# Kernel optimization log

Hardware: AMD Instinct MI355X
Metric: run time of the kernel (lower is better)

Reference implementation:

```python
import jax, jax.numpy as jnp
import numpy as np

NE, NM, D = 10000, 2048, 128
LEVELS = 6  # levels arg 5 -> self.levels = 6 relation types


def setup_inputs() -> dict:
    key = jax.random.key(0)
    ks = jax.random.split(key, 9)
    s = 0.05
    return {
        "emb_entity": jax.random.normal(ks[0], (1, NE, D), jnp.float32),
        "emb_mole": jax.random.normal(ks[1], (1, NM, D), jnp.float32),
        "entity_mole_weight": jax.random.uniform(ks[2], (NE, NM), jnp.float32),
        "W1": jax.random.normal(ks[3], (LEVELS, D, D), jnp.float32) * s,
        "root1": jax.random.normal(ks[4], (D, D), jnp.float32) * s,
        "b1": jax.random.normal(ks[5], (D,), jnp.float32) * s,
        "W2": jax.random.normal(ks[6], (LEVELS, D, D), jnp.float32) * s,
        "root2": jax.random.normal(ks[7], (D, D), jnp.float32) * s,
        "b2": jax.random.normal(ks[8], (D,), jnp.float32) * s,
    }


def reference(emb_entity, emb_mole, entity_mole_weight, W1, root1, b1, W2, root2, b2):
    x_e = emb_entity[0]  # [NE, D]
    x_m = emb_mole[0]    # [NM, D]
    # weight w in (i/LEVELS, (i+1)/LEVELS]  <=>  ceil(w*LEVELS) - 1 == i ; only i=1..LEVELS-1 form edges
    lev = jnp.ceil(entity_mole_weight * LEVELS).astype(jnp.int32) - 1  # [NE, NM]

    def rel_agg(x_src, W):
        # RGCN mean aggregation per relation type (edges Mole -> Entity), summed over relations
        out = jnp.zeros((x_e.shape[0], W.shape[-1]), x_src.dtype)
        for r in range(1, LEVELS):
            mask = (lev == r).astype(x_src.dtype)          # [NE, NM] relation-r adjacency
            cnt = mask.sum(axis=1, keepdims=True)          # in-degree per entity for relation r
            inv = jnp.where(cnt > 0, 1.0 / cnt, 0.0)
            out = out + ((mask @ x_src) * inv) @ W[r]      # mean message then relation transform
        return out

    # conv1 over homogeneous graph [Entity; Mole]; moles receive no edges -> root+bias only
    e1 = x_e @ root1 + rel_agg(x_m, W1) + b1
    m1 = x_m @ root1 + b1
    e1 = jax.nn.relu(e1)
    m1 = jax.nn.relu(m1)
    # conv2; only the entity slice of the output is returned
    e2 = e1 @ root2 + rel_agg(m1, W2) + b2
    return e2[None]  # [1, NE, D]
```

## Files before the change

### kernel.cpp

```cpp
#include <hip/hip_runtime.h>
#include <stdint.h>


#define NE 10000
#define NM 2048
#define NEPAD 10112
#define MB128 79
#define KSPLIT 16

typedef short bf8_t __attribute__((ext_vector_type(8)));
typedef float f16f  __attribute__((ext_vector_type(16)));

__device__ __forceinline__ uint16_t f2bf(float f){
  uint32_t u = __float_as_uint(f);
  u += 0x7FFFu + ((u >> 16) & 1u);
  return (uint16_t)(u >> 16);
}

__device__ __forceinline__ f16f mfma32(bf8_t a, bf8_t b, f16f c){
  return __builtin_amdgcn_mfma_f32_32x32x16_bf16(a, b, c, 0, 0, 0);
}

__global__ __launch_bounds__(256) void k_init(
    const float* __restrict__ root1, const float* __restrict__ root2,
    const float* __restrict__ W1, const float* __restrict__ W2,
    uint16_t* __restrict__ r1t, uint16_t* __restrict__ r2t,
    uint16_t* __restrict__ w1t, uint16_t* __restrict__ w2t,
    const float* __restrict__ w, const float* __restrict__ xe,
    uint32_t* __restrict__ levq, float* __restrict__ inv,
    uint16_t* __restrict__ xebf){
  int t = threadIdx.x;
  if (blockIdx.x < 48){
    int idx = blockIdx.x*4096 + t;
    #pragma unroll
    for (int it = 0; it < 16; it++, idx += 256){
      int slab = idx >> 14;
      int pos  = idx & 16383;
      int d = pos >> 7, k = pos & 127;
      float v; uint16_t* dst;
      if (slab == 0)      { v = root1[k*128 + d]; dst = r1t; }
      else if (slab == 1) { v = root2[k*128 + d]; dst = r2t; }
      else if (slab < 7)  { v = W1[(slab-1)*16384 + k*128 + d]; dst = w1t + (slab-2)*16384; }
      else                { v = W2[(slab-6)*16384 + k*128 + d]; dst = w2t + (slab-7)*16384; }
      dst[pos] = f2bf(v);
    }
    return;
  }
  int brow = (blockIdx.x - 48) * 32;
  int rloc = t >> 3, p = t & 7;
  int row = brow + rloc;
  bool active = row < NE;
  const float* wr = w + (size_t)row * NM;
  unsigned long long cnt = 0ull;
  __shared__ uint32_t tile[32][33];

  for (int cp = 0; cp < 8; cp++){
    uint32_t packs[4];
    #pragma unroll
    for (int q = 0; q < 4; q++){
      int gck = cp*32 + p + 8*q;
      uint32_t L = 0;
      if (active){
        const float4* f = (const float4*)(wr + gck*8);
        float4 f0 = f[0], f1 = f[1];
        float wv[8] = {f0.x,f0.y,f0.z,f0.w, f1.x,f1.y,f1.z,f1.w};
        #pragma unroll
        for (int e = 0; e < 8; e++){
          int s = (int)ceilf(wv[e]*6.0f);
          if (s >= 2) cnt += 1ull << (12*(s-2));
          L |= (uint32_t)s << (4*e);
        }
      }
      packs[q] = L;
    }
    __syncthreads();
    #pragma unroll
    for (int q = 0; q < 4; q++) tile[p + 8*q][rloc] = packs[q];
    __syncthreads();
    int ckk = t >> 3;
    int r4  = (t & 7) * 4;
    size_t base = (size_t)(cp*32 + ckk) * NEPAD + brow + r4;
    *(uint4*)(levq + base) = make_uint4(tile[ckk][r4], tile[ckk][r4+1],
                                        tile[ckk][r4+2], tile[ckk][r4+3]);
  }

  unsigned long long c = cnt;
  c += __shfl_xor(c, 1);
  c += __shfl_xor(c, 2);
  c += __shfl_xor(c, 4);
  if (p == 0 && row < NEPAD){
    if (active){
      inv[row*8 + 0] = 0.f; inv[row*8 + 6] = 0.f; inv[row*8 + 7] = 0.f;
      #pragma unroll
      for (int r = 1; r <= 5; r++){
        uint32_t cc = (uint32_t)((c >> (12*(r-1))) & 0xFFFull);
        inv[row*8 + r] = cc ? 1.0f/(float)cc : 0.f;
      }
    } else {
      #pragma unroll
      for (int i = 0; i < 8; i++) inv[row*8 + i] = 0.f;
    }
  }

  int f0i = p * 16;
  if (active){
    union { uint16_t u[16]; uint4 q[2]; } ub;
    #pragma unroll
    for (int j = 0; j < 4; j++){
      float4 a = *(const float4*)(xe + (size_t)row*128 + f0i + j*4);
      ub.u[j*4+0]=f2bf(a.x); ub.u[j*4+1]=f2bf(a.y); ub.u[j*4+2]=f2bf(a.z); ub.u[j*4+3]=f2bf(a.w);
    }
    *(uint4*)(xebf + (size_t)row*128 + f0i)     = ub.q[0];
    *(uint4*)(xebf + (size_t)row*128 + f0i + 8) = ub.q[1];
  } else if (row < NEPAD){
    uint4 z = make_uint4(0,0,0,0);
    *(uint4*)(xebf + (size_t)row*128 + f0i)     = z;
    *(uint4*)(xebf + (size_t)row*128 + f0i + 8) = z;
  }
}

__global__ __launch_bounds__(256) void k_gemm(
    const float* __restrict__ Af, const uint16_t* __restrict__ Bm,
    const uint16_t* __restrict__ Bz, const float* __restrict__ bias,
    uint16_t* __restrict__ m1out, uint16_t* __restrict__ zpk){
  int tid = threadIdx.x;
  int lane = tid & 63, wid = tid >> 6;
  int l31 = lane & 31, g = lane >> 5;
  int by = blockIdx.y;
  bool m1path = (by == 0);
  int r = by - 1;
  const uint16_t* B = m1path ? Bm : (Bz + (size_t)r*16384);
  int arow = blockIdx.x*128 + wid*32 + l31;

  f16f acc[4];
  #pragma unroll
  for (int n = 0; n < 4; n++)
    #pragma unroll
    for (int i = 0; i < 16; i++) acc[n][i] = 0.f;

  #pragma unroll
  for (int ksI = 0; ksI < 8; ksI++){
    int k0 = ksI*16 + g*8;
    const float* ap = Af + (size_t)arow*128 + k0;
    float4 f0 = *(const float4*)ap;
    float4 f1 = *(const float4*)(ap + 4);
    union { uint16_t u[8]; bf8_t v; } ua;
    ua.u[0]=f2bf(f0.x); ua.u[1]=f2bf(f0.y); ua.u[2]=f2bf(f0.z); ua.u[3]=f2bf(f0.w);
    ua.u[4]=f2bf(f1.x); ua.u[5]=f2bf(f1.y); ua.u[6]=f2bf(f1.z); ua.u[7]=f2bf(f1.w);
    #pragma unroll
    for (int n = 0; n < 4; n++){
      bf8_t b = *(const bf8_t*)(B + (size_t)(n*32 + l31)*128 + k0);
      acc[n] = mfma32(ua.v, b, acc[n]);
    }
  }
  #pragma unroll
  for (int n = 0; n < 4; n++){
    int colg = n*32 + l31;
    float bv = m1path ? bias[colg] : 0.f;
    #pragma unroll
    for (int v = 0; v < 16; v++){
      int rowl = (v&3) + 8*(v>>2) + 4*g;
      int rg = blockIdx.x*128 + wid*32 + rowl;
      float val = acc[n][v];
      if (m1path){
        m1out[(size_t)rg*128 + colg] = f2bf(fmaxf(val + bv, 0.f));
      } else {
        int pos = ((rg & 1) << 2) | ((rg & 7) >> 1);
        zpk[(size_t)(r*256 + (rg>>3))*1024 + colg*8 + pos] = f2bf(val);
      }
    }
  }
}

template<bool S16, bool ROOT>
__device__ __forceinline__ void conv_core(
    const uint32_t* __restrict__ levq, const float* __restrict__ inv,
    const uint16_t* __restrict__ zpk, const uint16_t* __restrict__ aroot,
    const uint16_t* __restrict__ rt,
    uint16_t* __restrict__ p16, float* __restrict__ p32,
    int tid){
  int lane = tid & 63, wid = tid >> 6;
  int l31 = lane & 31, g = lane >> 5;
  int wm = wid >> 1, wn = wid & 1;
  int bx = blockIdx.x;
  int brow = bx*128;
  int ks = blockIdx.y;
  int kc0 = ks*16;
  int rowA = brow + wm*64 + l31;
  int rowB = rowA + 32;
  int colb = wn*64;

  uint32_t LA[8], LB[8];
  #pragma unroll
  for (int j = 0; j < 8; j++){
    int kt = kc0 + ((j + bx) & 7)*2 + g;
    LA[j] = levq[(size_t)kt*NEPAD + rowA];
    LB[j] = levq[(size_t)kt*NEPAD + rowB];
  }

  uint32_t tlo[2][5], thi[2][5];
  #pragma unroll
  for (int mt = 0; mt < 2; mt++){
    int rg = mt ? rowB : rowA;
    #pragma unroll
    for (int r = 1; r <= 5; r++){
      uint32_t bits = (uint32_t)f2bf(inv[(size_t)rg*8 + r]);
      int sh = 8*((r+1)&3);
      tlo[mt][r-1] = (bits & 0xFFu) << sh;
      thi[mt][r-1] = (bits >> 8)    << sh;
    }
  }

  f16f acc[2][2];
  #pragma unroll
  for (int a0=0;a0<2;a0++)
    #pragma unroll
    for (int b0=0;b0<2;b0++)
      #pragma unroll
      for (int i=0;i<16;i++) acc[a0][b0][i]=0.f;

  if (ROOT && ks < 8){
    int k0 = ks*16 + g*8;
    bf8_t a0 = *(const bf8_t*)(aroot + (size_t)rowA*128 + k0);
    bf8_t a1 = *(const bf8_t*)(aroot + (size_t)rowB*128 + k0);
    #pragma unroll
    for (int nt = 0; nt < 2; nt++){
      bf8_t rb = *(const bf8_t*)(rt + (size_t)(colb + nt*32 + l31)*128 + k0);
      acc[0][nt] = mfma32(a0, rb, acc[0][nt]);
      acc[1][nt] = mfma32(a1, rb, acc[1][nt]);
    }
  }

  #pragma unroll
  for (int kk = 0; kk < 8; kk++){
    int kt = kc0 + ((kk + bx) & 7)*2 + g;
    uint32_t sxA = LA[kk] & 0x0F0F0F0Fu, syA = (LA[kk] >> 4) & 0x0F0F0F0Fu;
    uint32_t sxB = LB[kk] & 0x0F0F0F0Fu, syB = (LB[kk] >> 4) & 0x0F0F0F0Fu;
    const uint16_t* zb = zpk + (size_t)kt*1024 + (size_t)(colb + l31)*8;
    #pragma unroll
    for (int r = 1; r <= 5; r++){
      const uint16_t* zr = zb + (size_t)(r-1)*262144;
      bf8_t bn0 = *(const bf8_t*)(zr);
      bf8_t bn1 = *(const bf8_t*)(zr + 256);
      #pragma unroll
      for (int mt = 0; mt < 2; mt++){
        uint32_t sx = mt ? sxB : sxA;
        uint32_t sy = mt ? syB : syA;
        uint32_t TL = tlo[mt][r-1], TH = thi[mt][r-1];
        uint32_t pl, ph, ql, qh;
        if (r < 3){
          pl = __builtin_amdgcn_perm(0u, TL, sx);
          ph = __builtin_amdgcn_perm(0u, TH, sx);
          ql = __builtin_amdgcn_perm(0u, TL, sy);
          qh = __builtin_amdgcn_perm(0u, TH, sy);
        } else {
          pl = __builtin_amdgcn_perm(TL, 0u, sx);
          ph = __builtin_amdgcn_perm(TH, 0u, sx);
          ql = __builtin_amdgcn_perm(TL, 0u, sy);
          qh = __builtin_amdgcn_perm(TH, 0u, sy);
        }
        union { uint32_t u[4]; bf8_t v; } A;
        A.u[0] = __builtin_amdgcn_perm(ph, pl, 0x05010400u);
        A.u[1] = __builtin_amdgcn_perm(ph, pl, 0x07030602u);
        A.u[2] = __builtin_amdgcn_perm(qh, ql, 0x05010400u);
        A.u[3] = __builtin_amdgcn_perm(qh, ql, 0x07030602u);
        acc[mt][0] = mfma32(A.v, bn0, acc[mt][0]);
        acc[mt][1] = mfma32(A.v, bn1, acc[mt][1]);
      }
    }
  }

  if (S16){
    uint16_t* dst = p16 + (size_t)ks*NEPAD*128;
    #pragma unroll
    for (int mt = 0; mt < 2; mt++){
      #pragma unroll
      for (int nt = 0; nt < 2; nt++){
        int colg = colb + nt*32 + l31;
        #pragma unroll
        for (int v = 0; v < 16; v++){
          int rowl = (v&3) + 8*(v>>2) + 4*g;
          dst[(size_t)(brow + wm*64 + mt*32 + rowl)*128 + colg] = f2bf(acc[mt][nt][v]);
        }
      }
    }
  } else {
    #pragma unroll
    for (int mt = 0; mt < 2; mt++){
      #pragma unroll
      for (int nt = 0; nt < 2; nt++){
        int colg = colb + nt*32 + l31;
        #pragma unroll
        for (int v = 0; v < 16; v++){
          int rowl = (v&3) + 8*(v>>2) + 4*g;
          unsafeAtomicAdd(&p32[(size_t)(brow + wm*64 + mt*32 + rowl)*128 + colg],
                          acc[mt][nt][v]);
        }
      }
    }
  }
}

template<bool S16>
__global__ __launch_bounds__(256, 3) void k_convA(
    const uint32_t* __restrict__ levq, const float* __restrict__ inv,
    const uint16_t* __restrict__ zpk, const uint16_t* __restrict__ aroot,
    const uint16_t* __restrict__ rt,
    const uint16_t* __restrict__ gA, const uint16_t* __restrict__ gB,
    uint16_t* __restrict__ gOut,
    uint16_t* __restrict__ p16, float* __restrict__ p32){
  int tid = threadIdx.x;
  int lane = tid & 63, wid = tid >> 6;
  int l31 = lane & 31, g = lane >> 5;

  if (blockIdx.x >= MB128){
    int b = blockIdx.y*5 + (blockIdx.x - MB128);
    int r = b >> 4;
    int rowb = (b & 15)*128 + wid*32;
    int arow = rowb + l31;
    const uint16_t* B = gB + (size_t)r*16384;
    f16f acc[4];
    #pragma unroll
    for (int n = 0; n < 4; n++)
      #pragma unroll
      for (int i = 0; i < 16; i++) acc[n][i] = 0.f;
    #pragma unroll
    for (int ksI = 0; ksI < 8; ksI++){
      int k0 = ksI*16 + g*8;
      bf8_t a = *(const bf8_t*)(gA + (size_t)arow*128 + k0);
      #pragma unroll
      for (int n = 0; n < 4; n++){
        bf8_t bb = *(const bf8_t*)(B + (size_t)(n*32 + l31)*128 + k0);
        acc[n] = mfma32(a, bb, acc[n]);
      }
    }
    #pragma unroll
    for (int n = 0; n < 4; n++){
      int colg = n*32 + l31;
      #pragma unroll
      for (int v = 0; v < 16; v++){
        int rowl = (v&3) + 8*(v>>2) + 4*g;
        int rg = rowb + rowl;
        int pos = ((rg & 1) << 2) | ((rg & 7) >> 1);
        gOut[(size_t)(r*256 + (rg>>3))*1024 + colg*8 + pos] = f2bf(acc[n][v]);
      }
    }
    return;
  }
  conv_core<S16, true>(levq, inv, zpk, aroot, rt, p16, p32, tid);
}

template<bool S16>
__global__ __launch_bounds__(256, 3) void k_convB(
    const uint32_t* __restrict__ levq, const float* __restrict__ inv,
    const uint16_t* __restrict__ zpk,
    const uint16_t* __restrict__ pA16, const float* __restrict__ pA32,
    const uint16_t* __restrict__ rt, const float* __restrict__ b1,
    uint16_t* __restrict__ pB16, float* __restrict__ pB32,
    float* __restrict__ rootslab){
  __shared__ uint16_t e1s[128*136];
  int tid = threadIdx.x;
  int lane = tid & 63, wid = tid >> 6;
  int l31 = lane & 31, g = lane >> 5;

  if (blockIdx.x >= MB128){
    int rid = blockIdx.y*5 + (blockIdx.x - MB128);
    if (rid >= MB128) return;
    #pragma unroll
    for (int c = 0; c < 8; c++){
      int eo = c*2048 + tid*8;
      size_t base = (size_t)rid*16384 + eo;
      int col = eo & 127;
      float s[8];
      float4 bv0 = *(const float4*)(b1 + col);
      float4 bv1 = *(const float4*)(b1 + col + 4);
      s[0]=bv0.x; s[1]=bv0.y; s[2]=bv0.z; s[3]=bv0.w;
      s[4]=bv1.x; s[5]=bv1.y; s[6]=bv1.z; s[7]=bv1.w;
      if (S16){
        #pragma unroll
        for (int sl = 0; sl < KSPLIT; sl++){
          union { uint4 q; uint16_t h[8]; } u;
          u.q = *(const uint4*)(pA16 + (size_t)sl*NEPAD*128 + base);
          #pragma unroll
          for (int j = 0; j < 8; j++) s[j] += __uint_as_float(((uint32_t)u.h[j]) << 16);
        }
      } else {
        #pragma unroll
        for (int j = 0; j < 8; j += 4){
          float4 v = *(const float4*)(pA32 + base + j);
          s[j] += v.x; s[j+1] += v.y; s[j+2] += v.z; s[j+3] += v.w;
        }
      }
      union { uint16_t u[8]; uint4 q; } ub;
      #pragma unroll
      for (int j = 0; j < 8; j++) ub.u[j] = f2bf(fmaxf(s[j], 0.f));
      int row = eo >> 7;
      *(uint4*)(&e1s[row*136 + col]) = ub.q;
    }
    __syncthreads();
    f16f racc[4];
    #pragma unroll
    for (int n = 0; n < 4; n++)
      #pragma unroll
      for (int i = 0; i < 16; i++) racc[n][i] = 0.f;
    #pragma unroll
    for (int kk = 0; kk < 8; kk++){
      int k0 = kk*16 + g*8;
      bf8_t a = *(const bf8_t*)(&e1s[(wid*32 + l31)*136 + k0]);
      #pragma unroll
      for (int n = 0; n < 4; n++){
        bf8_t b = *(const bf8_t*)(rt + (size_t)(n*32 + l31)*128 + k0);
        racc[n] = mfma32(a, b, racc[n]);
      }
    }
    #pragma unroll
    for (int n = 0; n < 4; n++){
      int colg = n*32 + l31;
      #pragma unroll
      for (int v = 0; v < 16; v++){
        int rowl = (v&3) + 8*(v>>2) + 4*g;
        rootslab[(size_t)(rid*128 + wid*32 + rowl)*128 + colg] = racc[n][v];
      }
    }
    return;
  }
  conv_core<S16, false>(levq, inv, zpk, (const uint16_t*)nullptr, rt, pB16, pB32, tid);
}

template<bool S16>
__global__ __launch_bounds__(256) void k_red2(
    const uint16_t* __restrict__ pB16, const float* __restrict__ pB32,
    const float* __restrict__ rootslab, const float* __restrict__ b2,
    float* __restrict__ out){
  size_t idx8 = ((size_t)blockIdx.x*256 + threadIdx.x) * 8;
  if (idx8 >= (size_t)NE*128) return;
  int col = (int)(idx8 & 127);
  float s[8];
  float4 bv0 = *(const float4*)(b2 + col);
  float4 bv1 = *(const float4*)(b2 + col + 4);
  s[0]=bv0.x; s[1]=bv0.y; s[2]=bv0.z; s[3]=bv0.w;
  s[4]=bv1.x; s[5]=bv1.y; s[6]=bv1.z; s[7]=bv1.w;
  float4 r0 = *(const float4*)(rootslab + idx8);
  float4 r1 = *(const float4*)(rootslab + idx8 + 4);
  s[0]+=r0.x; s[1]+=r0.y; s[2]+=r0.z; s[3]+=r0.w;
  s[4]+=r1.x; s[5]+=r1.y; s[6]+=r1.z; s[7]+=r1.w;
  if (S16){
    #pragma unroll
    for (int sl = 0; sl < KSPLIT; sl++){
      union { uint4 q; uint16_t h[8]; } u;
      u.q = *(const uint4*)(pB16 + (size_t)sl*NEPAD*128 + idx8);
      #pragma unroll
      for (int j = 0; j < 8; j++) s[j] += __uint_as_float(((uint32_t)u.h[j]) << 16);
    }
  } else {
    #pragma unroll
    for (int j = 0; j < 8; j += 4){
      float4 v = *(const float4*)(pB32 + idx8 + j);
      s[j] += v.x; s[j+1] += v.y; s[j+2] += v.z; s[j+3] += v.w;
    }
  }
  *(float4*)(out + idx8)     = make_float4(s[0], s[1], s[2], s[3]);
  *(float4*)(out + idx8 + 4) = make_float4(s[4], s[5], s[6], s[7]);
}

extern "C" void kernel_launch(void* const* d_in, const int* in_sizes, int n_in,
                              void* d_out, int out_size, void* d_ws, size_t ws_size,
                              hipStream_t stream){
  const float* xe  = (const float*)d_in[0];
  const float* xm  = (const float*)d_in[1];
  const float* w   = (const float*)d_in[2];
  const float* W1  = (const float*)d_in[3];
  const float* r1  = (const float*)d_in[4];
  const float* b1  = (const float*)d_in[5];
  const float* W2  = (const float*)d_in[6];
  const float* r2  = (const float*)d_in[7];
  const float* b2  = (const float*)d_in[8];
  float* out = (float*)d_out;
  char* ws = (char*)d_ws;

  constexpr size_t OFF_INV  = 0;
  constexpr size_t OFF_XEBF = OFF_INV  + (size_t)NEPAD*8*4;
  constexpr size_t OFF_M1   = OFF_XEBF + (size_t)NEPAD*128*2;
  constexpr size_t OFF_Z1   = OFF_M1   + (size_t)NM*128*2;
  constexpr size_t OFF_Z2   = OFF_Z1   + (size_t)5*NM*128*2;
  constexpr size_t OFF_R1T  = OFF_Z2   + (size_t)5*NM*128*2;
  constexpr size_t OFF_R2T  = OFF_R1T  + 128*128*2;
  constexpr size_t OFF_W1T  = OFF_R2T  + 128*128*2;
  constexpr size_t OFF_W2T  = OFF_W1T  + (size_t)5*128*128*2;
  constexpr size_t OFF_LEVQ = OFF_W2T  + (size_t)5*128*128*2;
  constexpr size_t OFF_PA   = OFF_LEVQ + (size_t)256*NEPAD*4;
  constexpr size_t SLAB16   = (size_t)NEPAD*128*2;
  constexpr size_t SLABF    = (size_t)NEPAD*128*4;
  constexpr size_t OFF_PB   = OFF_PA   + (size_t)KSPLIT*SLAB16;
  constexpr size_t OFF_ROOT = OFF_PB   + (size_t)KSPLIT*SLAB16;
  constexpr size_t NEED_A   = OFF_ROOT + SLABF;
  constexpr size_t OFF_PB_B   = OFF_PA + SLABF;
  constexpr size_t OFF_ROOT_B = OFF_PB_B + SLABF;
  constexpr size_t NEED_B     = OFF_ROOT_B + SLABF;

  float*    inv  = (float*)   (ws + OFF_INV);
  uint16_t* xebf = (uint16_t*)(ws + OFF_XEBF);
  uint16_t* m1   = (uint16_t*)(ws + OFF_M1);
  uint16_t* z1   = (uint16_t*)(ws + OFF_Z1);
  uint16_t* z2   = (uint16_t*)(ws + OFF_Z2);
  uint16_t* r1t  = (uint16_t*)(ws + OFF_R1T);
  uint16_t* r2t  = (uint16_t*)(ws + OFF_R2T);
  uint16_t* w1t  = (uint16_t*)(ws + OFF_W1T);
  uint16_t* w2t  = (uint16_t*)(ws + OFF_W2T);
  uint32_t* levq = (uint32_t*)(ws + OFF_LEVQ);

  bool tierA = (ws_size >= NEED_A);

  hipLaunchKernelGGL(k_init, dim3(48 + NEPAD/32), dim3(256), 0, stream,
                     r1, r2, W1, W2, r1t, r2t, w1t, w2t,
                     w, xe, levq, inv, xebf);
  hipLaunchKernelGGL(k_gemm, dim3(16,6), dim3(256), 0, stream,
                     xm, r1t, w1t, b1, m1, z1);
  if (tierA){
    uint16_t* pA   = (uint16_t*)(ws + OFF_PA);
    uint16_t* pB   = (uint16_t*)(ws + OFF_PB);
    float*    root = (float*)   (ws + OFF_ROOT);
    hipLaunchKernelGGL((k_convA<true>), dim3(MB128 + 5, KSPLIT), dim3(256), 0, stream,
                       levq, inv, z1, xebf, r1t, m1, w2t, z2,
                       pA, (float*)nullptr);
    hipLaunchKernelGGL((k_convB<true>), dim3(MB128 + 5, KSPLIT), dim3(256), 0, stream,
                       levq, inv, z2, pA, (const float*)nullptr, r2t, b1,
                       pB, (float*)nullptr, root);
    hipLaunchKernelGGL((k_red2<true>), dim3((NE*128 + 2047)/2048), dim3(256), 0, stream,
                       pB, (const float*)nullptr, root, b2, out);
  } else {
    float* pA   = (float*)(ws + OFF_PA);
    float* pB   = (float*)(ws + OFF_PB_B);
    float* root = (float*)(ws + OFF_ROOT_B);
    hipMemsetAsync(pA, 0, SLABF, stream);
    hipMemsetAsync(pB, 0, SLABF, stream);
    hipLaunchKernelGGL((k_convA<false>), dim3(MB128 + 5, KSPLIT), dim3(256), 0, stream,
                       levq, inv, z1, xebf, r1t, m1, w2t, z2,
                       (uint16_t*)nullptr, pA);
    hipLaunchKernelGGL((k_convB<false>), dim3(MB128 + 5, KSPLIT), dim3(256), 0, stream,
                       levq, inv, z2, (const uint16_t*)nullptr, pA, r2t, b1,
                       (uint16_t*)nullptr, pB, root);
    hipLaunchKernelGGL((k_red2<false>), dim3((NE*128 + 2047)/2048), dim3(256), 0, stream,
                       (const uint16_t*)nullptr, pB, root, b2, out);
  }
}
```

Before: 127.9 us.

## Fuse mole GEMM into init kernel and read fp32 weights directly

Drops the separate weight-transpose/bf16 conversion pass and the standalone k_gemm launch. The mole-side GEMMs (m1 and the z1 relation products) now run as extra blocks inside k_init. All consumers read fp32 root/W matrices straight from the inputs, gathering strided columns and converting to bf16 on the fly. The intent is to save one kernel launch and a pass over weight memory. In exchange, B-operand loads become strided scalar reads with per-element conversion. The conv kernels also get a lower occupancy hint (2 instead of 3) and drop the per-block k-tile rotation.

```diff
diff --git a/kernel.cpp b/kernel.cpp
--- a/kernel.cpp
+++ b/kernel.cpp
@@ -22,31 +22,69 @@
 }
 
 __global__ __launch_bounds__(256) void k_init(
-    const float* __restrict__ root1, const float* __restrict__ root2,
-    const float* __restrict__ W1, const float* __restrict__ W2,
-    uint16_t* __restrict__ r1t, uint16_t* __restrict__ r2t,
-    uint16_t* __restrict__ w1t, uint16_t* __restrict__ w2t,
     const float* __restrict__ w, const float* __restrict__ xe,
+    const float* __restrict__ xm, const float* __restrict__ root1,
+    const float* __restrict__ W1, const float* __restrict__ b1,
     uint32_t* __restrict__ levq, float* __restrict__ inv,
-    uint16_t* __restrict__ xebf){
+    uint16_t* __restrict__ xebf, uint16_t* __restrict__ m1,
+    uint16_t* __restrict__ z1){
   int t = threadIdx.x;
-  if (blockIdx.x < 48){
-    int idx = blockIdx.x*4096 + t;
-    #pragma unroll
-    for (int it = 0; it < 16; it++, idx += 256){
-      int slab = idx >> 14;
-      int pos  = idx & 16383;
-      int d = pos >> 7, k = pos & 127;
-      float v; uint16_t* dst;
-      if (slab == 0)      { v = root1[k*128 + d]; dst = r1t; }
-      else if (slab == 1) { v = root2[k*128 + d]; dst = r2t; }
-      else if (slab < 7)  { v = W1[(slab-1)*16384 + k*128 + d]; dst = w1t + (slab-2)*16384; }
-      else                { v = W2[(slab-6)*16384 + k*128 + d]; dst = w2t + (slab-7)*16384; }
-      dst[pos] = f2bf(v);
+  int lane = t & 63, wid = t >> 6;
+  int l31 = lane & 31, g = lane >> 5;
+
+  if (blockIdx.x >= 316){
+    int gb = blockIdx.x - 316;
+    int gbx = gb & 15, gby = gb >> 4;
+    bool m1path = (gby == 0);
+    const float* Bsrc = m1path ? root1 : (W1 + (size_t)gby*16384);
+    int arow = gbx*128 + wid*32 + l31;
+
+    f16f acc[4];
+    #pragma unroll
+    for (int n = 0; n < 4; n++)
+      #pragma unroll
+      for (int i = 0; i < 16; i++) acc[n][i] = 0.f;
+
+    #pragma unroll
+    for (int ksI = 0; ksI < 8; ksI++){
+      int k0 = ksI*16 + g*8;
+      const float* ap = xm + (size_t)arow*128 + k0;
+      float4 f0 = *(const float4*)ap;
+      float4 f1 = *(const float4*)(ap + 4);
+      union { uint16_t u[8]; bf8_t v; } ua;
+      ua.u[0]=f2bf(f0.x); ua.u[1]=f2bf(f0.y); ua.u[2]=f2bf(f0.z); ua.u[3]=f2bf(f0.w);
+      ua.u[4]=f2bf(f1.x); ua.u[5]=f2bf(f1.y); ua.u[6]=f2bf(f1.z); ua.u[7]=f2bf(f1.w);
+      #pragma unroll
+      for (int n = 0; n < 4; n++){
+        int d = n*32 + l31;
+        union { uint16_t u[8]; bf8_t v; } ub;
+        #pragma unroll
+        for (int e = 0; e < 8; e++)
+          ub.u[e] = f2bf(Bsrc[(size_t)(k0+e)*128 + d]);
+        acc[n] = mfma32(ua.v, ub.v, acc[n]);
+      }
+    }
+    #pragma unroll
+    for (int n = 0; n < 4; n++){
+      int colg = n*32 + l31;
+      float bv = m1path ? b1[colg] : 0.f;
+      #pragma unroll
+      for (int v = 0; v < 16; v++){
+        int rowl = (v&3) + 8*(v>>2) + 4*g;
+        int rg = gbx*128 + wid*32 + rowl;
+        float val = acc[n][v];
+        if (m1path){
+          m1[(size_t)rg*128 + colg] = f2bf(fmaxf(val + bv, 0.f));
+        } else {
+          int pos = ((rg & 1) << 2) | ((rg & 7) >> 1);
+          z1[(size_t)((gby-1)*256 + (rg>>3))*1024 + colg*8 + pos] = f2bf(val);
+        }
+      }
     }
     return;
   }
-  int brow = (blockIdx.x - 48) * 32;
+
+  int brow = blockIdx.x * 32;
   int rloc = t >> 3, p = t & 7;
   int row = brow + rloc;
   bool active = row < NE;
@@ -119,71 +157,16 @@
   }
 }
 
-__global__ __launch_bounds__(256) void k_gemm(
-    const float* __restrict__ Af, const uint16_t* __restrict__ Bm,
-    const uint16_t* __restrict__ Bz, const float* __restrict__ bias,
-    uint16_t* __restrict__ m1out, uint16_t* __restrict__ zpk){
-  int tid = threadIdx.x;
-  int lane = tid & 63, wid = tid >> 6;
-  int l31 = lane & 31, g = lane >> 5;
-  int by = blockIdx.y;
-  bool m1path = (by == 0);
-  int r = by - 1;
-  const uint16_t* B = m1path ? Bm : (Bz + (size_t)r*16384);
-  int arow = blockIdx.x*128 + wid*32 + l31;
-
-  f16f acc[4];
-  #pragma unroll
-  for (int n = 0; n < 4; n++)
-    #pragma unroll
-    for (int i = 0; i < 16; i++) acc[n][i] = 0.f;
-
-  #pragma unroll
-  for (int ksI = 0; ksI < 8; ksI++){
-    int k0 = ksI*16 + g*8;
-    const float* ap = Af + (size_t)arow*128 + k0;
-    float4 f0 = *(const float4*)ap;
-    float4 f1 = *(const float4*)(ap + 4);
-    union { uint16_t u[8]; bf8_t v; } ua;
-    ua.u[0]=f2bf(f0.x); ua.u[1]=f2bf(f0.y); ua.u[2]=f2bf(f0.z); ua.u[3]=f2bf(f0.w);
-    ua.u[4]=f2bf(f1.x); ua.u[5]=f2bf(f1.y); ua.u[6]=f2bf(f1.z); ua.u[7]=f2bf(f1.w);
-    #pragma unroll
-    for (int n = 0; n < 4; n++){
-      bf8_t b = *(const bf8_t*)(B + (size_t)(n*32 + l31)*128 + k0);
-      acc[n] = mfma32(ua.v, b, acc[n]);
-    }
-  }
-  #pragma unroll
-  for (int n = 0; n < 4; n++){
-    int colg = n*32 + l31;
-    float bv = m1path ? bias[colg] : 0.f;
-    #pragma unroll
-    for (int v = 0; v < 16; v++){
-      int rowl = (v&3) + 8*(v>>2) + 4*g;
-      int rg = blockIdx.x*128 + wid*32 + rowl;
-      float val = acc[n][v];
-      if (m1path){
-        m1out[(size_t)rg*128 + colg] = f2bf(fmaxf(val + bv, 0.f));
-      } else {
-        int pos = ((rg & 1) << 2) | ((rg & 7) >> 1);
-        zpk[(size_t)(r*256 + (rg>>3))*1024 + colg*8 + pos] = f2bf(val);
-      }
-    }
-  }
-}
-
 template<bool S16, bool ROOT>
 __device__ __forceinline__ void conv_core(
     const uint32_t* __restrict__ levq, const float* __restrict__ inv,
     const uint16_t* __restrict__ zpk, const uint16_t* __restrict__ aroot,
-    const uint16_t* __restrict__ rt,
-    uint16_t* __restrict__ p16, float* __restrict__ p32,
-    int tid){
+    const float* __restrict__ rootf,
+    uint16_t* __restrict__ p16, float* __restrict__ p32, int tid){
   int lane = tid & 63, wid = tid >> 6;
   int l31 = lane & 31, g = lane >> 5;
   int wm = wid >> 1, wn = wid & 1;
-  int bx = blockIdx.x;
-  int brow = bx*128;
+  int brow = blockIdx.x*128;
   int ks = blockIdx.y;
   int kc0 = ks*16;
   int rowA = brow + wm*64 + l31;
@@ -192,10 +175,10 @@
 
   uint32_t LA[8], LB[8];
   #pragma unroll
-  for (int j = 0; j < 8; j++){
-    int kt = kc0 + ((j + bx) & 7)*2 + g;
-    LA[j] = levq[(size_t)kt*NEPAD + rowA];
-    LB[j] = levq[(size_t)kt*NEPAD + rowB];
+  for (int kk = 0; kk < 8; kk++){
+    int kt = kc0 + kk*2 + g;
+    LA[kk] = levq[(size_t)kt*NEPAD + rowA];
+    LB[kk] = levq[(size_t)kt*NEPAD + rowB];
   }
 
   uint32_t tlo[2][5], thi[2][5];
@@ -225,15 +208,19 @@
     bf8_t a1 = *(const bf8_t*)(aroot + (size_t)rowB*128 + k0);
     #pragma unroll
     for (int nt = 0; nt < 2; nt++){
-      bf8_t rb = *(const bf8_t*)(rt + (size_t)(colb + nt*32 + l31)*128 + k0);
-      acc[0][nt] = mfma32(a0, rb, acc[0][nt]);
-      acc[1][nt] = mfma32(a1, rb, acc[1][nt]);
+      int d = colb + nt*32 + l31;
+      union { uint16_t u[8]; bf8_t v; } ub;
+      #pragma unroll
+      for (int e = 0; e < 8; e++)
+        ub.u[e] = f2bf(rootf[(size_t)(k0+e)*128 + d]);
+      acc[0][nt] = mfma32(a0, ub.v, acc[0][nt]);
+      acc[1][nt] = mfma32(a1, ub.v, acc[1][nt]);
     }
   }
 
   #pragma unroll
   for (int kk = 0; kk < 8; kk++){
-    int kt = kc0 + ((kk + bx) & 7)*2 + g;
+    int kt = kc0 + kk*2 + g;
     uint32_t sxA = LA[kk] & 0x0F0F0F0Fu, syA = (LA[kk] >> 4) & 0x0F0F0F0Fu;
     uint32_t sxB = LB[kk] & 0x0F0F0F0Fu, syB = (LB[kk] >> 4) & 0x0F0F0F0Fu;
     const uint16_t* zb = zpk + (size_t)kt*1024 + (size_t)(colb + l31)*8;
@@ -302,23 +289,23 @@
 }
 
 template<bool S16>
-__global__ __launch_bounds__(256, 3) void k_convA(
+__global__ __launch_bounds__(256, 2) void k_convA(
     const uint32_t* __restrict__ levq, const float* __restrict__ inv,
-    const uint16_t* __restrict__ zpk, const uint16_t* __restrict__ aroot,
-    const uint16_t* __restrict__ rt,
-    const uint16_t* __restrict__ gA, const uint16_t* __restrict__ gB,
-    uint16_t* __restrict__ gOut,
+    const uint16_t* __restrict__ z1, const uint16_t* __restrict__ xebf,
+    const float* __restrict__ root1,
+    const uint16_t* __restrict__ m1, const float* __restrict__ W2,
+    uint16_t* __restrict__ z2,
     uint16_t* __restrict__ p16, float* __restrict__ p32){
   int tid = threadIdx.x;
   int lane = tid & 63, wid = tid >> 6;
   int l31 = lane & 31, g = lane >> 5;
 
   if (blockIdx.x >= MB128){
-    int b = blockIdx.y*5 + (blockIdx.x - MB128);
-    int r = b >> 4;
-    int rowb = (b & 15)*128 + wid*32;
+    int fb = blockIdx.y*5 + (blockIdx.x - MB128);
+    int r = fb >> 4;
+    int rowb = (fb & 15)*128 + wid*32;
     int arow = rowb + l31;
-    const uint16_t* B = gB + (size_t)r*16384;
+    const float* Bsrc = W2 + (size_t)(r+1)*16384;
     f16f acc[4];
     #pragma unroll
     for (int n = 0; n < 4; n++)
@@ -327,11 +314,15 @@
     #pragma unroll
     for (int ksI = 0; ksI < 8; ksI++){
       int k0 = ksI*16 + g*8;
-      bf8_t a = *(const bf8_t*)(gA + (size_t)arow*128 + k0);
+      bf8_t a = *(const bf8_t*)(m1 + (size_t)arow*128 + k0);
       #pragma unroll
       for (int n = 0; n < 4; n++){
-        bf8_t bb = *(const bf8_t*)(B + (size_t)(n*32 + l31)*128 + k0);
-        acc[n] = mfma32(a, bb, acc[n]);
+        int d = n*32 + l31;
+        union { uint16_t u[8]; bf8_t v; } ub;
+        #pragma unroll
+        for (int e = 0; e < 8; e++)
+          ub.u[e] = f2bf(Bsrc[(size_t)(k0+e)*128 + d]);
+        acc[n] = mfma32(a, ub.v, acc[n]);
       }
     }
     #pragma unroll
@@ -342,20 +333,20 @@
         int rowl = (v&3) + 8*(v>>2) + 4*g;
         int rg = rowb + rowl;
         int pos = ((rg & 1) << 2) | ((rg & 7) >> 1);
-        gOut[(size_t)(r*256 + (rg>>3))*1024 + colg*8 + pos] = f2bf(acc[n][v]);
+        z2[(size_t)(r*256 + (rg>>3))*1024 + colg*8 + pos] = f2bf(acc[n][v]);
       }
     }
     return;
   }
-  conv_core<S16, true>(levq, inv, zpk, aroot, rt, p16, p32, tid);
+  conv_core<S16, true>(levq, inv, z1, xebf, root1, p16, p32, tid);
 }
 
 template<bool S16>
-__global__ __launch_bounds__(256, 3) void k_convB(
+__global__ __launch_bounds__(256, 2) void k_convB(
     const uint32_t* __restrict__ levq, const float* __restrict__ inv,
-    const uint16_t* __restrict__ zpk,
+    const uint16_t* __restrict__ z2,
     const uint16_t* __restrict__ pA16, const float* __restrict__ pA32,
-    const uint16_t* __restrict__ rt, const float* __restrict__ b1,
+    const float* __restrict__ root2, const float* __restrict__ b1,
     uint16_t* __restrict__ pB16, float* __restrict__ pB32,
     float* __restrict__ rootslab){
   __shared__ uint16_t e1s[128*136];
@@ -409,8 +400,12 @@
       bf8_t a = *(const bf8_t*)(&e1s[(wid*32 + l31)*136 + k0]);
       #pragma unroll
       for (int n = 0; n < 4; n++){
-        bf8_t b = *(const bf8_t*)(rt + (size_t)(n*32 + l31)*128 + k0);
-        racc[n] = mfma32(a, b, racc[n]);
+        int d = n*32 + l31;
+        union { uint16_t u[8]; bf8_t v; } ub;
+        #pragma unroll
+        for (int e = 0; e < 8; e++)
+          ub.u[e] = f2bf(root2[(size_t)(k0+e)*128 + d]);
+        racc[n] = mfma32(a, ub.v, racc[n]);
       }
     }
     #pragma unroll
@@ -424,7 +419,8 @@
     }
     return;
   }
-  conv_core<S16, false>(levq, inv, zpk, (const uint16_t*)nullptr, rt, pB16, pB32, tid);
+  conv_core<S16, false>(levq, inv, z2, (const uint16_t*)nullptr,
+                        (const float*)nullptr, pB16, pB32, tid);
 }
 
 template<bool S16>
@@ -483,11 +479,7 @@
   constexpr size_t OFF_M1   = OFF_XEBF + (size_t)NEPAD*128*2;
   constexpr size_t OFF_Z1   = OFF_M1   + (size_t)NM*128*2;
   constexpr size_t OFF_Z2   = OFF_Z1   + (size_t)5*NM*128*2;
-  constexpr size_t OFF_R1T  = OFF_Z2   + (size_t)5*NM*128*2;
-  constexpr size_t OFF_R2T  = OFF_R1T  + 128*128*2;
-  constexpr size_t OFF_W1T  = OFF_R2T  + 128*128*2;
-  constexpr size_t OFF_W2T  = OFF_W1T  + (size_t)5*128*128*2;
-  constexpr size_t OFF_LEVQ = OFF_W2T  + (size_t)5*128*128*2;
+  constexpr size_t OFF_LEVQ = OFF_Z2   + (size_t)5*NM*128*2;
   constexpr size_t OFF_PA   = OFF_LEVQ + (size_t)256*NEPAD*4;
   constexpr size_t SLAB16   = (size_t)NEPAD*128*2;
   constexpr size_t SLABF    = (size_t)NEPAD*128*4;
@@ -496,35 +488,26 @@
   constexpr size_t NEED_A   = OFF_ROOT + SLABF;
   constexpr size_t OFF_PB_B   = OFF_PA + SLABF;
   constexpr size_t OFF_ROOT_B = OFF_PB_B + SLABF;
-  constexpr size_t NEED_B     = OFF_ROOT_B + SLABF;
 
   float*    inv  = (float*)   (ws + OFF_INV);
   uint16_t* xebf = (uint16_t*)(ws + OFF_XEBF);
   uint16_t* m1   = (uint16_t*)(ws + OFF_M1);
   uint16_t* z1   = (uint16_t*)(ws + OFF_Z1);
   uint16_t* z2   = (uint16_t*)(ws + OFF_Z2);
-  uint16_t* r1t  = (uint16_t*)(ws + OFF_R1T);
-  uint16_t* r2t  = (uint16_t*)(ws + OFF_R2T);
-  uint16_t* w1t  = (uint16_t*)(ws + OFF_W1T);
-  uint16_t* w2t  = (uint16_t*)(ws + OFF_W2T);
   uint32_t* levq = (uint32_t*)(ws + OFF_LEVQ);
 
   bool tierA = (ws_size >= NEED_A);
 
-  hipLaunchKernelGGL(k_init, dim3(48 + NEPAD/32), dim3(256), 0, stream,
-                     r1, r2, W1, W2, r1t, r2t, w1t, w2t,
-                     w, xe, levq, inv, xebf);
-  hipLaunchKernelGGL(k_gemm, dim3(16,6), dim3(256), 0, stream,
-                     xm, r1t, w1t, b1, m1, z1);
+  hipLaunchKernelGGL(k_init, dim3(316 + 96), dim3(256), 0, stream,
+                     w, xe, xm, r1, W1, b1, levq, inv, xebf, m1, z1);
   if (tierA){
     uint16_t* pA   = (uint16_t*)(ws + OFF_PA);
     uint16_t* pB   = (uint16_t*)(ws + OFF_PB);
     float*    root = (float*)   (ws + OFF_ROOT);
     hipLaunchKernelGGL((k_convA<true>), dim3(MB128 + 5, KSPLIT), dim3(256), 0, stream,
-                       levq, inv, z1, xebf, r1t, m1, w2t, z2,
-                       pA, (float*)nullptr);
+                       levq, inv, z1, xebf, r1, m1, W2, z2, pA, (float*)nullptr);
     hipLaunchKernelGGL((k_convB<true>), dim3(MB128 + 5, KSPLIT), dim3(256), 0, stream,
-                       levq, inv, z2, pA, (const float*)nullptr, r2t, b1,
+                       levq, inv, z2, pA, (const float*)nullptr, r2, b1,
                        pB, (float*)nullptr, root);
     hipLaunchKernelGGL((k_red2<true>), dim3((NE*128 + 2047)/2048), dim3(256), 0, stream,
                        pB, (const float*)nullptr, root, b2, out);
@@ -535,10 +518,9 @@
     hipMemsetAsync(pA, 0, SLABF, stream);
     hipMemsetAsync(pB, 0, SLABF, stream);
     hipLaunchKernelGGL((k_convA<false>), dim3(MB128 + 5, KSPLIT), dim3(256), 0, stream,
-                       levq, inv, z1, xebf, r1t, m1, w2t, z2,
-                       (uint16_t*)nullptr, pA);
+                       levq, inv, z1, xebf, r1, m1, W2, z2, (uint16_t*)nullptr, pA);
     hipLaunchKernelGGL((k_convB<false>), dim3(MB128 + 5, KSPLIT), dim3(256), 0, stream,
-                       levq, inv, z2, (const uint16_t*)nullptr, pA, r2t, b1,
+                       levq, inv, z2, (const uint16_t*)nullptr, pA, r2, b1,
                        (uint16_t*)nullptr, pB, root);
     hipLaunchKernelGGL((k_red2<false>), dim3((NE*128 + 2047)/2048), dim3(256), 0, stream,
                        (const uint16_t*)nullptr, pB, root, b2, out);
```

Result: faster. 110.1 us (-13.9%).
